# Optimization experiments

Measured on AMD Instinct MI355X. Metric: run time of the kernel, lower is better.

Reference implementation:

```python
import jax, jax.numpy as jnp
import numpy as np

N = 100000      # nodes
E = 1600000     # graph edges (avg degree 16)
Q = 1000000     # query edges to score
IN, HID, OUT = 128, 128, 64


def setup_inputs() -> dict:
    key = jax.random.key(0)
    ks = jax.random.split(key, 7)
    feat = jax.random.normal(ks[0], (N, IN), dtype=jnp.float32)
    edge_src = jax.random.randint(ks[1], (E,), 0, N, dtype=jnp.int32)
    edge_dst = jax.random.randint(ks[2], (E,), 0, N, dtype=jnp.int32)
    src = jax.random.randint(ks[3], (Q,), 0, N, dtype=jnp.int32)
    dst = jax.random.randint(ks[4], (Q,), 0, N, dtype=jnp.int32)
    W1 = jax.random.normal(ks[5], (IN, HID), dtype=jnp.float32) / np.sqrt(IN).astype(np.float32)
    b1 = jnp.zeros((HID,), jnp.float32)
    W2 = jax.random.normal(ks[6], (HID, OUT), dtype=jnp.float32) / np.sqrt(HID).astype(np.float32)
    b2 = jnp.zeros((OUT,), jnp.float32)
    return {"feat": feat, "edge_src": edge_src, "edge_dst": edge_dst,
            "src": src, "dst": dst, "W1": W1, "b1": b1, "W2": W2, "b2": b2}


def _graph_conv(h, W, b, edge_src, edge_dst, out_norm, in_norm):
    """DGL GraphConv(norm='both'): D_out^{-1/2} -> aggregate -> D_in^{-1/2}, W, b.
    DGL applies W before aggregation when in_feats > out_feats (same math)."""
    n = h.shape[0]
    h = h * out_norm[:, None]
    if h.shape[1] > W.shape[1]:
        h = h @ W
        agg = jax.ops.segment_sum(h[edge_src], edge_dst, num_segments=n)
    else:
        agg = jax.ops.segment_sum(h[edge_src], edge_dst, num_segments=n)
        agg = agg @ W
    return agg * in_norm[:, None] + b


def reference(feat, edge_src, edge_dst, src, dst, W1, b1, W2, b2):
    n = feat.shape[0]
    ones = jnp.ones((edge_src.shape[0],), feat.dtype)
    out_deg = jax.ops.segment_sum(ones, edge_src, num_segments=n)
    in_deg = jax.ops.segment_sum(ones, edge_dst, num_segments=n)
    out_norm = jnp.maximum(out_deg, 1.0) ** -0.5
    in_norm = jnp.maximum(in_deg, 1.0) ** -0.5

    h = _graph_conv(feat, W1, b1, edge_src, edge_dst, out_norm, in_norm)
    h = jax.nn.relu(h)  # dropout is identity at inference
    h = _graph_conv(h, W2, b2, edge_src, edge_dst, out_norm, in_norm)

    edge_scores = jnp.sum(h[src] * h[dst], axis=-1)
    return jax.nn.sigmoid(edge_scores)
```

## Files before the change

kernel.cpp:

```cpp
#include <hip/hip_runtime.h>
#include <math.h>

static inline size_t align256(size_t x) { return (x + 255) & ~(size_t)255; }

typedef __attribute__((ext_vector_type(8))) short bf16x8;
typedef __attribute__((ext_vector_type(4))) float f32x4;

__device__ inline float bfLo(unsigned int u) {
  union { unsigned int i; float f; } v; v.i = u << 16; return v.f;
}
__device__ inline float bfHi(unsigned int u) {
  union { unsigned int i; float f; } v; v.i = u & 0xffff0000u; return v.f;
}
__device__ inline float bf2f(unsigned short u) {
  union { unsigned int i; float f; } v; v.i = ((unsigned int)u) << 16; return v.f;
}
__device__ inline unsigned short f2bf(float f) {
  union { float f; unsigned int i; } v; v.f = f;
  unsigned int r = v.i + 0x7FFF + ((v.i >> 16) & 1);
  return (unsigned short)(r >> 16);
}
__device__ inline unsigned int packbf(float lo, float hi) {
  return ((unsigned int)f2bf(hi) << 16) | f2bf(lo);
}

__global__ __launch_bounds__(256) void k_coarse_count(const int* __restrict__ esrc,
                                                      const int* __restrict__ edst,
                                                      int E, int chunk, int NB, int G,
                                                      int* __restrict__ blkD,
                                                      int* __restrict__ blkS,
                                                      const float* __restrict__ W1,
                                                      const float* __restrict__ W2,
                                                      unsigned short* __restrict__ W1t,
                                                      unsigned short* __restrict__ W2t) {
  __shared__ int hD[512], hS[512];
  int blk = blockIdx.x, tid = threadIdx.x;
  int t = blk * 256 + tid;
  if (t < 128 * 128) {
    int nn = t >> 7, kk = t & 127;
    W1t[t] = f2bf(W1[kk * 128 + nn]);
  }
  if (t < 64 * 128) {
    int nn = t >> 7, kk = t & 127;
    W2t[t] = f2bf(W2[kk * 64 + nn]);
  }
  for (int i = tid; i < NB; i += 256) { hD[i] = 0; hS[i] = 0; }
  __syncthreads();
  int s0 = blk * chunk, s1 = min(E, s0 + chunk);
  for (int e = s0 + tid; e < s1; e += 256) {
    atomicAdd(&hD[edst[e] >> 8], 1);
    atomicAdd(&hS[esrc[e] >> 8], 1);
  }
  __syncthreads();
  for (int i = tid; i < NB; i += 256) {
    blkD[i * G + blk] = hD[i];
    blkS[i * G + blk] = hS[i];
  }
}

__global__ __launch_bounds__(256) void k_scan1(const int* __restrict__ in,
                                               int* __restrict__ out,
                                               int* __restrict__ bsums, int n) {
  __shared__ int s[256];
  int tid = threadIdx.x, gid = blockIdx.x * 256 + tid;
  int v = (gid < n) ? in[gid] : 0;
  s[tid] = v; __syncthreads();
  for (int o = 1; o < 256; o <<= 1) {
    int t = (tid >= o) ? s[tid - o] : 0;
    __syncthreads();
    s[tid] += t;
    __syncthreads();
  }
  if (gid < n) out[gid] = s[tid] - v;
  if (tid == 255) bsums[blockIdx.x] = s[255];
}

__global__ __launch_bounds__(512) void k_scan2(int* __restrict__ bsums, int nb) {
  __shared__ int s[512];
  int tid = threadIdx.x;
  int* base = bsums + blockIdx.x * nb;
  int v = (tid < nb) ? base[tid] : 0;
  s[tid] = v; __syncthreads();
  for (int o = 1; o < 512; o <<= 1) {
    int t = (tid >= o) ? s[tid - o] : 0;
    __syncthreads();
    s[tid] += t;
    __syncthreads();
  }
  if (tid < nb) base[tid] = s[tid] - v;
}

__global__ __launch_bounds__(256) void k_coarse_scatter(const int* __restrict__ esrc,
                                                        const int* __restrict__ edst,
                                                        int E, int chunk, int NB, int G,
                                                        const int* __restrict__ scD,
                                                        const int* __restrict__ scS,
                                                        const int* __restrict__ bsums,
                                                        unsigned int* __restrict__ pairs,
                                                        unsigned int* __restrict__ keys) {
  __shared__ int cD[512], cS[512];
  int blk = blockIdx.x, tid = threadIdx.x;
  for (int i = tid; i < NB; i += 256) {
    cD[i] = scD[i * G + blk] + bsums[i];
    cS[i] = scS[i * G + blk] + bsums[NB + i];
  }
  __syncthreads();
  int s0 = blk * chunk, s1 = min(E, s0 + chunk);
  for (int e = s0 + tid; e < s1; e += 256) {
    int s = esrc[e], d = edst[e];
    int pd = atomicAdd(&cD[d >> 8], 1);
    pairs[pd] = ((unsigned)s << 8) | ((unsigned)d & 255u);
    int ps = atomicAdd(&cS[s >> 8], 1);
    keys[ps] = (unsigned)s;
  }
}

__global__ __launch_bounds__(256) void k_fine(const unsigned int* __restrict__ pairs,
                                              const unsigned int* __restrict__ keys,
                                              const int* __restrict__ scD,
                                              const int* __restrict__ scS,
                                              const int* __restrict__ bsums,
                                              int G, int E, int N, int NB,
                                              int* __restrict__ cntIn,
                                              float* __restrict__ normIn,
                                              int* __restrict__ offs,
                                              int* __restrict__ csr,
                                              float* __restrict__ normOut) {
  __shared__ int hist[256], scn[256], cur[256];
  int tid = threadIdx.x;
  if (blockIdx.x >= (unsigned)NB) {
    int b = blockIdx.x - NB;
    int bstart = scS[b * G] + bsums[NB + b];
    int bend = (b + 1 < NB) ? scS[(b + 1) * G] + bsums[NB + b + 1] : E;
    hist[tid] = 0;
    __syncthreads();
    for (int e = bstart + tid; e < bend; e += 256)
      atomicAdd(&hist[keys[e] & 255u], 1);
    __syncthreads();
    int node = b * 256 + tid;
    if (node < N) normOut[node] = rsqrtf((float)max(hist[tid], 1));
    return;
  }
  int b = blockIdx.x;
  int bstart = scD[b * G] + bsums[b];
  int bend = (b + 1 < NB) ? scD[(b + 1) * G] + bsums[b + 1] : E;
  hist[tid] = 0;
  __syncthreads();
  for (int e = bstart + tid; e < bend; e += 256)
    atomicAdd(&hist[pairs[e] & 255u], 1);
  __syncthreads();
  int v = hist[tid];
  scn[tid] = v;
  __syncthreads();
  for (int o = 1; o < 256; o <<= 1) {
    int t = (tid >= o) ? scn[tid - o] : 0;
    __syncthreads();
    scn[tid] += t;
    __syncthreads();
  }
  int excl = scn[tid] - v;
  cur[tid] = excl;
  int node = b * 256 + tid;
  if (node < N) {
    cntIn[node] = v;
    normIn[node] = rsqrtf((float)max(v, 1));
    offs[node] = bstart + excl;
  }
  __syncthreads();
  for (int e = bstart + tid; e < bend; e += 256) {
    unsigned int u = pairs[e];
    int p = bstart + atomicAdd(&cur[u & 255u], 1);
    csr[p] = (int)(u >> 8);
  }
}

template <int C, typename TA>
__global__ __launch_bounds__(256) void k_mgemm(const TA* __restrict__ A,
                                               const float* __restrict__ scale,
                                               const unsigned short* __restrict__ Wt,
                                               unsigned short* __restrict__ out, int n) {
  constexpr int KP = 136;
  constexpr int NCH = C / 16;
  __shared__ __align__(16) unsigned short Al[64 * KP];
  __shared__ __align__(16) unsigned short Wl[C * KP];
  int tid = threadIdx.x;
  int r0 = blockIdx.x * 64;

  {
    const uint4* Wg = (const uint4*)Wt;
    uint4* Wd = (uint4*)Wl;
    for (int idx = tid; idx < C * 16; idx += 256) {
      int row = idx >> 4, seg = idx & 15;
      Wd[row * 17 + seg] = Wg[idx];
    }
  }
  {
    int seg = tid & 7;
    for (int it = 0; it < 2; ++it) {
      int row = (tid >> 3) + it * 32;
      int g = r0 + row;
      float v[16];
      if (g < n) {
        float sc = scale[g];
        if constexpr (sizeof(TA) == 4) {
          const float4* Ag = (const float4*)((const float*)A + (size_t)g * 128);
#pragma unroll
          for (int j = 0; j < 4; ++j) {
            float4 f = Ag[seg * 4 + j];
            v[j * 4 + 0] = f.x * sc; v[j * 4 + 1] = f.y * sc;
            v[j * 4 + 2] = f.z * sc; v[j * 4 + 3] = f.w * sc;
          }
        } else {
          const uint4* Ag = (const uint4*)((const unsigned short*)A + (size_t)g * 128);
#pragma unroll
          for (int j = 0; j < 2; ++j) {
            uint4 u = Ag[seg * 2 + j];
            v[j * 8 + 0] = bfLo(u.x) * sc; v[j * 8 + 1] = bfHi(u.x) * sc;
            v[j * 8 + 2] = bfLo(u.y) * sc; v[j * 8 + 3] = bfHi(u.y) * sc;
            v[j * 8 + 4] = bfLo(u.z) * sc; v[j * 8 + 5] = bfHi(u.z) * sc;
            v[j * 8 + 6] = bfLo(u.w) * sc; v[j * 8 + 7] = bfHi(u.w) * sc;
          }
        }
      } else {
#pragma unroll
        for (int j = 0; j < 16; ++j) v[j] = 0.f;
      }
      uint4* dst = (uint4*)(Al + row * KP + seg * 16);
      dst[0] = make_uint4(packbf(v[0], v[1]), packbf(v[2], v[3]),
                          packbf(v[4], v[5]), packbf(v[6], v[7]));
      dst[1] = make_uint4(packbf(v[8], v[9]), packbf(v[10], v[11]),
                          packbf(v[12], v[13]), packbf(v[14], v[15]));
    }
  }
  __syncthreads();

  int lane = tid & 63;
  int w = tid >> 6;
  int quad = lane >> 4, m16 = lane & 15;
  f32x4 acc[NCH];
#pragma unroll
  for (int c = 0; c < NCH; ++c) acc[c] = (f32x4){0.f, 0.f, 0.f, 0.f};

#pragma unroll
  for (int kc = 0; kc < 4; ++kc) {
    int ko = kc * 32 + quad * 8;
    bf16x8 a = *(const bf16x8*)(Al + (w * 16 + m16) * KP + ko);
#pragma unroll
    for (int c = 0; c < NCH; ++c) {
      bf16x8 b = *(const bf16x8*)(Wl + (c * 16 + m16) * KP + ko);
      acc[c] = __builtin_amdgcn_mfma_f32_16x16x32_bf16(a, b, acc[c], 0, 0, 0);
    }
  }

#pragma unroll
  for (int c = 0; c < NCH; ++c)
#pragma unroll
    for (int r = 0; r < 4; ++r) {
      int g = r0 + w * 16 + quad * 4 + r;
      if (g < n) out[(size_t)g * C + c * 16 + m16] = f2bf(acc[c][r]);
    }
}

__global__ __launch_bounds__(256) void k_agg128h(const unsigned short* __restrict__ X,
                                                 const int* __restrict__ csr,
                                                 const int* __restrict__ offs,
                                                 const int* __restrict__ cnt,
                                                 const float* __restrict__ norm,
                                                 const float* __restrict__ bias,
                                                 unsigned short* __restrict__ H, int n) {
  int b = blockIdx.x;
  int xcd = b & 7;
  int half = xcd >> 2;
  int grpIdx = (b >> 3) * 4 + (xcd & 3);
  int wid = grpIdx * 4 + (threadIdx.x >> 6);
  if (wid >= n) return;
  int lane = threadIdx.x & 63;
  int sub = lane & 7;
  int grp = lane >> 3;
  int hoff = half * 8;
  int start = offs[wid], m = cnt[wid];
  const int* p = csr + start;
  const uint4* Xv = (const uint4*)X;
  float a[8] = {0.f, 0.f, 0.f, 0.f, 0.f, 0.f, 0.f, 0.f};
  for (int c0 = 0; c0 < m; c0 += 64) {
    int take = min(64, m - c0);
    int iv = p[c0 + ((lane < take) ? lane : take - 1)];
    int e = 0;
    for (; e + 32 <= take; e += 32) {
      uint4 uu[4];
#pragma unroll
      for (int j = 0; j < 4; ++j) {
        int ss = __shfl(iv, e + j * 8 + grp);
        uu[j] = Xv[(size_t)ss * 16 + hoff + sub];
      }
#pragma unroll
      for (int j = 0; j < 4; ++j) {
        a[0] += bfLo(uu[j].x); a[1] += bfHi(uu[j].x);
        a[2] += bfLo(uu[j].y); a[3] += bfHi(uu[j].y);
        a[4] += bfLo(uu[j].z); a[5] += bfHi(uu[j].z);
        a[6] += bfLo(uu[j].w); a[7] += bfHi(uu[j].w);
      }
    }
    for (; e + 8 <= take; e += 8) {
      int ss = __shfl(iv, e + grp);
      uint4 u = Xv[(size_t)ss * 16 + hoff + sub];
      a[0] += bfLo(u.x); a[1] += bfHi(u.x);
      a[2] += bfLo(u.y); a[3] += bfHi(u.y);
      a[4] += bfLo(u.z); a[5] += bfHi(u.z);
      a[6] += bfLo(u.w); a[7] += bfHi(u.w);
    }
    int r = take - e;
    if (r > 0) {
      int ss = __shfl(iv, min(e + grp, take - 1));
      uint4 u = Xv[(size_t)ss * 16 + hoff + sub];
      if (grp < r) {
        a[0] += bfLo(u.x); a[1] += bfHi(u.x);
        a[2] += bfLo(u.y); a[3] += bfHi(u.y);
        a[4] += bfLo(u.z); a[5] += bfHi(u.z);
        a[6] += bfLo(u.w); a[7] += bfHi(u.w);
      }
    }
  }
#pragma unroll
  for (int k = 0; k < 8; ++k) {
    a[k] += __shfl_xor(a[k], 8);
    a[k] += __shfl_xor(a[k], 16);
    a[k] += __shfl_xor(a[k], 32);
  }
  float nm = norm[wid];
  const float4* bv = (const float4*)bias;
  float4 b0 = bv[half * 16 + sub * 2], b1 = bv[half * 16 + sub * 2 + 1];
  if (grp == 0) {
    float o0 = fmaxf(a[0] * nm + b0.x, 0.f);
    float o1 = fmaxf(a[1] * nm + b0.y, 0.f);
    float o2 = fmaxf(a[2] * nm + b0.z, 0.f);
    float o3 = fmaxf(a[3] * nm + b0.w, 0.f);
    float o4 = fmaxf(a[4] * nm + b1.x, 0.f);
    float o5 = fmaxf(a[5] * nm + b1.y, 0.f);
    float o6 = fmaxf(a[6] * nm + b1.z, 0.f);
    float o7 = fmaxf(a[7] * nm + b1.w, 0.f);
    uint4 o = make_uint4(packbf(o0, o1), packbf(o2, o3),
                         packbf(o4, o5), packbf(o6, o7));
    ((uint4*)H)[(size_t)wid * 16 + hoff + sub] = o;
  }
}

__global__ __launch_bounds__(256) void k_agg64(const unsigned short* __restrict__ X,
                                               const int* __restrict__ csr,
                                               const int* __restrict__ offs,
                                               const int* __restrict__ cnt,
                                               const float* __restrict__ norm,
                                               const float* __restrict__ bias,
                                               unsigned short* __restrict__ H, int n) {
  int wid = blockIdx.x * 4 + (threadIdx.x >> 6);
  if (wid >= n) return;
  int lane = threadIdx.x & 63;
  int sub = lane & 7;
  int grp = lane >> 3;
  int start = offs[wid], m = cnt[wid];
  const int* p = csr + start;
  const uint4* Xv = (const uint4*)X;
  float a[8] = {0.f, 0.f, 0.f, 0.f, 0.f, 0.f, 0.f, 0.f};
  for (int c0 = 0; c0 < m; c0 += 64) {
    int take = min(64, m - c0);
    int iv = p[c0 + ((lane < take) ? lane : take - 1)];
    int e = 0;
    for (; e + 32 <= take; e += 32) {
      uint4 uu[4];
#pragma unroll
      for (int j = 0; j < 4; ++j) {
        int ss = __shfl(iv, e + j * 8 + grp);
        uu[j] = Xv[(size_t)ss * 8 + sub];
      }
#pragma unroll
      for (int j = 0; j < 4; ++j) {
        a[0] += bfLo(uu[j].x); a[1] += bfHi(uu[j].x);
        a[2] += bfLo(uu[j].y); a[3] += bfHi(uu[j].y);
        a[4] += bfLo(uu[j].z); a[5] += bfHi(uu[j].z);
        a[6] += bfLo(uu[j].w); a[7] += bfHi(uu[j].w);
      }
    }
    for (; e + 8 <= take; e += 8) {
      int ss = __shfl(iv, e + grp);
      uint4 u = Xv[(size_t)ss * 8 + sub];
      a[0] += bfLo(u.x); a[1] += bfHi(u.x);
      a[2] += bfLo(u.y); a[3] += bfHi(u.y);
      a[4] += bfLo(u.z); a[5] += bfHi(u.z);
      a[6] += bfLo(u.w); a[7] += bfHi(u.w);
    }
    int r = take - e;
    if (r > 0) {
      int ss = __shfl(iv, min(e + grp, take - 1));
      uint4 u = Xv[(size_t)ss * 8 + sub];
      if (grp < r) {
        a[0] += bfLo(u.x); a[1] += bfHi(u.x);
        a[2] += bfLo(u.y); a[3] += bfHi(u.y);
        a[4] += bfLo(u.z); a[5] += bfHi(u.z);
        a[6] += bfLo(u.w); a[7] += bfHi(u.w);
      }
    }
  }
#pragma unroll
  for (int k = 0; k < 8; ++k) {
    a[k] += __shfl_xor(a[k], 8);
    a[k] += __shfl_xor(a[k], 16);
    a[k] += __shfl_xor(a[k], 32);
  }
  float nm = norm[wid];
  const float4* bv = (const float4*)bias;
  float4 b0 = bv[sub * 2], b1 = bv[sub * 2 + 1];
  if (grp == 0) {
    uint4 o = make_uint4(packbf(a[0] * nm + b0.x, a[1] * nm + b0.y),
                         packbf(a[2] * nm + b0.z, a[3] * nm + b0.w),
                         packbf(a[4] * nm + b1.x, a[5] * nm + b1.y),
                         packbf(a[6] * nm + b1.z, a[7] * nm + b1.w));
    ((uint4*)H)[(size_t)wid * 8 + sub] = o;
  }
}

__global__ __launch_bounds__(256) void k_score(const unsigned short* __restrict__ H,
                                               const int* __restrict__ qs,
                                               const int* __restrict__ qd,
                                               float* __restrict__ out, int q) {
  int t = blockIdx.x * 256 + threadIdx.x;
  int sub = t & 7;
  int q0 = t >> 3;
  float p = 0.f;
  if (q0 < q) {
    int s = qs[q0], d = qd[q0];
    const uint4* Hv = (const uint4*)H;
    uint4 a = Hv[(size_t)s * 8 + sub];
    uint4 b = Hv[(size_t)d * 8 + sub];
    p = bfLo(a.x) * bfLo(b.x) + bfHi(a.x) * bfHi(b.x) +
        bfLo(a.y) * bfLo(b.y) + bfHi(a.y) * bfHi(b.y) +
        bfLo(a.z) * bfLo(b.z) + bfHi(a.z) * bfHi(b.z) +
        bfLo(a.w) * bfLo(b.w) + bfHi(a.w) * bfHi(b.w);
  }
  p += __shfl_xor(p, 1);
  p += __shfl_xor(p, 2);
  p += __shfl_xor(p, 4);
  if (sub == 0 && q0 < q) out[q0] = 1.f / (1.f + expf(-p));
}

extern "C" void kernel_launch(void* const* d_in, const int* in_sizes, int n_in,
                              void* d_out, int out_size, void* d_ws, size_t ws_size,
                              hipStream_t stream) {
  const float* feat = (const float*)d_in[0];
  const int* esrc   = (const int*)d_in[1];
  const int* edst   = (const int*)d_in[2];
  const int* qsrc   = (const int*)d_in[3];
  const int* qdst   = (const int*)d_in[4];
  const float* W1   = (const float*)d_in[5];
  const float* b1   = (const float*)d_in[6];
  const float* W2   = (const float*)d_in[7];
  const float* b2   = (const float*)d_in[8];
  float* out = (float*)d_out;

  const int N = in_sizes[0] / 128;
  const int E = in_sizes[1];
  const int Q = in_sizes[3];

  const int G = 256;
  const int NB = (N + 255) >> 8;
  const int chunk = (E + G - 1) / G;
  const int lenS = NB * G;
  const int gScan = lenS / 256;

  char* w = (char*)d_ws;
  size_t o = 0;
  unsigned short* X1 = (unsigned short*)(w + o); o += align256((size_t)N * 128 * 2);
  unsigned short* X2 = (unsigned short*)(w + o); o += align256((size_t)N * 64 * 2);
  unsigned short* H2 = (unsigned short*)(w + o); o += align256((size_t)N * 64 * 2);
  int* cntIn = (int*)(w + o);       o += align256((size_t)N * 4);
  float* normOut = (float*)(w + o); o += align256((size_t)N * 4);
  float* normIn = (float*)(w + o);  o += align256((size_t)N * 4);
  int* offs = (int*)(w + o);        o += align256((size_t)N * 4);
  int* blk = (int*)(w + o);         o += align256((size_t)lenS * 8);
  int* sc = (int*)(w + o);          o += align256((size_t)lenS * 8);
  int* bsums = (int*)(w + o);       o += align256((size_t)8192);
  unsigned short* W1t = (unsigned short*)(w + o); o += align256((size_t)128 * 128 * 2);
  unsigned short* W2t = (unsigned short*)(w + o); o += align256((size_t)64 * 128 * 2);
  unsigned int* pairs = (unsigned int*)(w + o); o += align256((size_t)E * 4);
  unsigned int* keys = (unsigned int*)(w + o); o += align256((size_t)E * 4);
  int* csr = (int*)(w + o);         o += align256((size_t)E * 4);

  int* blkD = blk;        int* blkS = blk + lenS;
  int* scD = sc;          int* scS = sc + lenS;

  k_coarse_count<<<G, 256, 0, stream>>>(esrc, edst, E, chunk, NB, G, blkD, blkS,
                                        W1, W2, W1t, W2t);
  k_scan1<<<2 * gScan, 256, 0, stream>>>(blk, sc, bsums, 2 * lenS);
  k_scan2<<<2, 512, 0, stream>>>(bsums, gScan);
  k_coarse_scatter<<<G, 256, 0, stream>>>(esrc, edst, E, chunk, NB, G, scD, scS,
                                          bsums, pairs, keys);
  k_fine<<<2 * NB, 256, 0, stream>>>(pairs, keys, scD, scS, bsums, G, E, N, NB,
                                     cntIn, normIn, offs, csr, normOut);

  const int gRows = (N + 63) / 64;
  const int nGrp4 = (N + 3) / 4;
  const int gAggH = 8 * ((nGrp4 + 3) / 4);
  k_mgemm<128, float><<<gRows, 256, 0, stream>>>(feat, normOut, W1t, X1, N);
  k_agg128h<<<gAggH, 256, 0, stream>>>(X1, csr, offs, cntIn, normIn, b1, X2, N);
  k_mgemm<64, unsigned short><<<gRows, 256, 0, stream>>>(X2, normOut, W2t, X1, N);
  k_agg64<<<(N + 3) / 4, 256, 0, stream>>>(X1, csr, offs, cntIn, normIn, b2, H2, N);
  k_score<<<((Q * 8) + 255) / 256, 256, 0, stream>>>(H2, qsrc, qdst, out, Q);
}
```

Baseline: 353.0 us.

## Use full-row 128-wide aggregation, deepen agg64 unroll, score two queries per thread

```diff
diff --git a/kernel.cpp b/kernel.cpp
--- a/kernel.cpp
+++ b/kernel.cpp
@@ -11,9 +11,6 @@
 }
 __device__ inline float bfHi(unsigned int u) {
   union { unsigned int i; float f; } v; v.i = u & 0xffff0000u; return v.f;
-}
-__device__ inline float bf2f(unsigned short u) {
-  union { unsigned int i; float f; } v; v.i = ((unsigned int)u) << 16; return v.f;
 }
 __device__ inline unsigned short f2bf(float f) {
   union { float f; unsigned int i; } v; v.f = f;
@@ -261,23 +258,18 @@
     }
 }
 
-__global__ __launch_bounds__(256) void k_agg128h(const unsigned short* __restrict__ X,
-                                                 const int* __restrict__ csr,
-                                                 const int* __restrict__ offs,
-                                                 const int* __restrict__ cnt,
-                                                 const float* __restrict__ norm,
-                                                 const float* __restrict__ bias,
-                                                 unsigned short* __restrict__ H, int n) {
-  int b = blockIdx.x;
-  int xcd = b & 7;
-  int half = xcd >> 2;
-  int grpIdx = (b >> 3) * 4 + (xcd & 3);
-  int wid = grpIdx * 4 + (threadIdx.x >> 6);
+__global__ __launch_bounds__(256) void k_agg128_relu(const unsigned short* __restrict__ X,
+                                                     const int* __restrict__ csr,
+                                                     const int* __restrict__ offs,
+                                                     const int* __restrict__ cnt,
+                                                     const float* __restrict__ norm,
+                                                     const float* __restrict__ bias,
+                                                     unsigned short* __restrict__ H, int n) {
+  int wid = blockIdx.x * 4 + (threadIdx.x >> 6);
   if (wid >= n) return;
   int lane = threadIdx.x & 63;
-  int sub = lane & 7;
-  int grp = lane >> 3;
-  int hoff = half * 8;
+  int sub = lane & 15;
+  int grp = lane >> 4;
   int start = offs[wid], m = cnt[wid];
   const int* p = csr + start;
   const uint4* Xv = (const uint4*)X;
@@ -287,23 +279,23 @@
     int iv = p[c0 + ((lane < take) ? lane : take - 1)];
     int e = 0;
     for (; e + 32 <= take; e += 32) {
-      uint4 uu[4];
-#pragma unroll
-      for (int j = 0; j < 4; ++j) {
-        int ss = __shfl(iv, e + j * 8 + grp);
-        uu[j] = Xv[(size_t)ss * 16 + hoff + sub];
-      }
-#pragma unroll
-      for (int j = 0; j < 4; ++j) {
+      uint4 uu[8];
+#pragma unroll
+      for (int j = 0; j < 8; ++j) {
+        int ss = __shfl(iv, e + j * 4 + grp);
+        uu[j] = Xv[(size_t)ss * 16 + sub];
+      }
+#pragma unroll
+      for (int j = 0; j < 8; ++j) {
         a[0] += bfLo(uu[j].x); a[1] += bfHi(uu[j].x);
         a[2] += bfLo(uu[j].y); a[3] += bfHi(uu[j].y);
         a[4] += bfLo(uu[j].z); a[5] += bfHi(uu[j].z);
         a[6] += bfLo(uu[j].w); a[7] += bfHi(uu[j].w);
       }
     }
-    for (; e + 8 <= take; e += 8) {
+    for (; e + 4 <= take; e += 4) {
       int ss = __shfl(iv, e + grp);
-      uint4 u = Xv[(size_t)ss * 16 + hoff + sub];
+      uint4 u = Xv[(size_t)ss * 16 + sub];
       a[0] += bfLo(u.x); a[1] += bfHi(u.x);
       a[2] += bfLo(u.y); a[3] += bfHi(u.y);
       a[4] += bfLo(u.z); a[5] += bfHi(u.z);
@@ -312,7 +304,7 @@
     int r = take - e;
     if (r > 0) {
       int ss = __shfl(iv, min(e + grp, take - 1));
-      uint4 u = Xv[(size_t)ss * 16 + hoff + sub];
+      uint4 u = Xv[(size_t)ss * 16 + sub];
       if (grp < r) {
         a[0] += bfLo(u.x); a[1] += bfHi(u.x);
         a[2] += bfLo(u.y); a[3] += bfHi(u.y);
@@ -323,13 +315,12 @@
   }
 #pragma unroll
   for (int k = 0; k < 8; ++k) {
-    a[k] += __shfl_xor(a[k], 8);
     a[k] += __shfl_xor(a[k], 16);
     a[k] += __shfl_xor(a[k], 32);
   }
   float nm = norm[wid];
   const float4* bv = (const float4*)bias;
-  float4 b0 = bv[half * 16 + sub * 2], b1 = bv[half * 16 + sub * 2 + 1];
+  float4 b0 = bv[sub * 2], b1 = bv[sub * 2 + 1];
   if (grp == 0) {
     float o0 = fmaxf(a[0] * nm + b0.x, 0.f);
     float o1 = fmaxf(a[1] * nm + b0.y, 0.f);
@@ -341,7 +332,7 @@
     float o7 = fmaxf(a[7] * nm + b1.w, 0.f);
     uint4 o = make_uint4(packbf(o0, o1), packbf(o2, o3),
                          packbf(o4, o5), packbf(o6, o7));
-    ((uint4*)H)[(size_t)wid * 16 + hoff + sub] = o;
+    ((uint4*)H)[(size_t)wid * 16 + sub] = o;
   }
 }
 
@@ -365,15 +356,15 @@
     int take = min(64, m - c0);
     int iv = p[c0 + ((lane < take) ? lane : take - 1)];
     int e = 0;
-    for (; e + 32 <= take; e += 32) {
-      uint4 uu[4];
-#pragma unroll
-      for (int j = 0; j < 4; ++j) {
+    for (; e + 64 <= take; e += 64) {
+      uint4 uu[8];
+#pragma unroll
+      for (int j = 0; j < 8; ++j) {
         int ss = __shfl(iv, e + j * 8 + grp);
         uu[j] = Xv[(size_t)ss * 8 + sub];
       }
 #pragma unroll
-      for (int j = 0; j < 4; ++j) {
+      for (int j = 0; j < 8; ++j) {
         a[0] += bfLo(uu[j].x); a[1] += bfHi(uu[j].x);
         a[2] += bfLo(uu[j].y); a[3] += bfHi(uu[j].y);
         a[4] += bfLo(uu[j].z); a[5] += bfHi(uu[j].z);
@@ -421,25 +412,39 @@
 __global__ __launch_bounds__(256) void k_score(const unsigned short* __restrict__ H,
                                                const int* __restrict__ qs,
                                                const int* __restrict__ qd,
-                                               float* __restrict__ out, int q) {
+                                               float* __restrict__ out, int q, int qStride) {
   int t = blockIdx.x * 256 + threadIdx.x;
   int sub = t & 7;
   int q0 = t >> 3;
-  float p = 0.f;
+  int q1 = q0 + qStride;
+  const uint4* Hv = (const uint4*)H;
+  float p0 = 0.f, p1 = 0.f;
   if (q0 < q) {
-    int s = qs[q0], d = qd[q0];
-    const uint4* Hv = (const uint4*)H;
-    uint4 a = Hv[(size_t)s * 8 + sub];
-    uint4 b = Hv[(size_t)d * 8 + sub];
-    p = bfLo(a.x) * bfLo(b.x) + bfHi(a.x) * bfHi(b.x) +
-        bfLo(a.y) * bfLo(b.y) + bfHi(a.y) * bfHi(b.y) +
-        bfLo(a.z) * bfLo(b.z) + bfHi(a.z) * bfHi(b.z) +
-        bfLo(a.w) * bfLo(b.w) + bfHi(a.w) * bfHi(b.w);
-  }
-  p += __shfl_xor(p, 1);
-  p += __shfl_xor(p, 2);
-  p += __shfl_xor(p, 4);
-  if (sub == 0 && q0 < q) out[q0] = 1.f / (1.f + expf(-p));
+    uint4 a = Hv[(size_t)qs[q0] * 8 + sub];
+    uint4 b = Hv[(size_t)qd[q0] * 8 + sub];
+    uint4 c, d;
+    bool has1 = (q1 < q);
+    if (has1) {
+      c = Hv[(size_t)qs[q1] * 8 + sub];
+      d = Hv[(size_t)qd[q1] * 8 + sub];
+    }
+    p0 = bfLo(a.x) * bfLo(b.x) + bfHi(a.x) * bfHi(b.x) +
+         bfLo(a.y) * bfLo(b.y) + bfHi(a.y) * bfHi(b.y) +
+         bfLo(a.z) * bfLo(b.z) + bfHi(a.z) * bfHi(b.z) +
+         bfLo(a.w) * bfLo(b.w) + bfHi(a.w) * bfHi(b.w);
+    if (has1)
+      p1 = bfLo(c.x) * bfLo(d.x) + bfHi(c.x) * bfHi(d.x) +
+           bfLo(c.y) * bfLo(d.y) + bfHi(c.y) * bfHi(d.y) +
+           bfLo(c.z) * bfLo(d.z) + bfHi(c.z) * bfHi(d.z) +
+           bfLo(c.w) * bfLo(d.w) + bfHi(c.w) * bfHi(d.w);
+  }
+  p0 += __shfl_xor(p0, 1); p1 += __shfl_xor(p1, 1);
+  p0 += __shfl_xor(p0, 2); p1 += __shfl_xor(p1, 2);
+  p0 += __shfl_xor(p0, 4); p1 += __shfl_xor(p1, 4);
+  if (sub == 0 && q0 < q) {
+    out[q0] = 1.f / (1.f + expf(-p0));
+    if (q1 < q) out[q1] = 1.f / (1.f + expf(-p1));
+  }
 }
 
 extern "C" void kernel_launch(void* const* d_in, const int* in_sizes, int n_in,
@@ -497,11 +502,10 @@
                                      cntIn, normIn, offs, csr, normOut);
 
   const int gRows = (N + 63) / 64;
-  const int nGrp4 = (N + 3) / 4;
-  const int gAggH = 8 * ((nGrp4 + 3) / 4);
   k_mgemm<128, float><<<gRows, 256, 0, stream>>>(feat, normOut, W1t, X1, N);
-  k_agg128h<<<gAggH, 256, 0, stream>>>(X1, csr, offs, cntIn, normIn, b1, X2, N);
+  k_agg128_relu<<<(N + 3) / 4, 256, 0, stream>>>(X1, csr, offs, cntIn, normIn, b1, X2, N);
   k_mgemm<64, unsigned short><<<gRows, 256, 0, stream>>>(X2, normOut, W2t, X1, N);
   k_agg64<<<(N + 3) / 4, 256, 0, stream>>>(X1, csr, offs, cntIn, normIn, b2, H2, N);
-  k_score<<<((Q * 8) + 255) / 256, 256, 0, stream>>>(H2, qsrc, qdst, out, Q);
-}
+  const int qHalf = (Q + 1) / 2;
+  k_score<<<((qHalf * 8) + 255) / 256, 256, 0, stream>>>(H2, qsrc, qdst, out, Q, qHalf);
+}
```

After: 373.8 us. 1.06x slower.
